# Optimization experiments

Hardware: AMD Instinct MI355X
Metric: run time of the kernel (lower is better)

Reference implementation:

```python
import jax, jax.numpy as jnp
import numpy as np

D_MODEL = 1024
D_HEAD = 128
BATCH = 4
SEQ = 4096


def setup_inputs() -> dict:
    key = jax.random.key(0)
    ks = jax.random.split(key, 7)
    s = 1.0 / np.sqrt(D_MODEL)
    return {
        "x": jax.random.normal(ks[0], (BATCH, SEQ, D_MODEL), dtype=jnp.float32),
        "Wq": jax.random.normal(ks[1], (D_MODEL, D_HEAD), dtype=jnp.float32) * s,
        "bq": jax.random.normal(ks[2], (D_HEAD,), dtype=jnp.float32) * 0.02,
        "Wk": jax.random.normal(ks[3], (D_MODEL, D_HEAD), dtype=jnp.float32) * s,
        "bk": jax.random.normal(ks[4], (D_HEAD,), dtype=jnp.float32) * 0.02,
        "Wv": jax.random.normal(ks[5], (D_MODEL, D_HEAD), dtype=jnp.float32) * s,
        "bv": jax.random.normal(ks[6], (D_HEAD,), dtype=jnp.float32) * 0.02,
    }


def reference(x, Wq, bq, Wk, bk, Wv, bv):
    # Single-head causal self-attention (intended math of MaskedAttention).
    # x: [B, S, D_MODEL]; projections to [B, S, D_HEAD].
    q = x @ Wq + bq
    k = x @ Wk + bk
    v = x @ Wv + bv
    scale = 1.0 / jnp.sqrt(jnp.asarray(D_HEAD, dtype=x.dtype))
    scores = jnp.einsum("bsd,btd->bst", q, k) * scale  # [B, S, S]
    # additive causal mask: -inf strictly above the diagonal
    s_len = scores.shape[-1]
    causal = jnp.tril(jnp.ones((s_len, s_len), dtype=bool))
    scores = jnp.where(causal[None, :, :], scores, jnp.asarray(-jnp.inf, dtype=scores.dtype))
    attn = jax.nn.softmax(scores, axis=-1)
    return jnp.einsum("bst,btd->bsd", attn, v)  # [B, S, D_HEAD]
```

## Files before the change

kernel.cpp:

```cpp
#include <hip/hip_runtime.h>
#include <stdint.h>
#include <stddef.h>

#define SEQ 4096
#define DM 1024
#define DH 128
#define NB 4
#define SPLITS 4

typedef __attribute__((ext_vector_type(8))) short bf16x8;
typedef __attribute__((ext_vector_type(4))) float f32x4;

__device__ __forceinline__ unsigned short f2bf(float f) {
    union { float f; uint32_t u; } v; v.f = f;
    uint32_t u = v.u + 0x7FFF + ((v.u >> 16) & 1);
    return (unsigned short)(u >> 16);
}

__device__ __forceinline__ void gload_lds16(const void* g, void* l) {
    __builtin_amdgcn_global_load_lds(
        (const __attribute__((address_space(1))) void*)g,
        (__attribute__((address_space(3))) void*)l, 16, 0, 0);
}

__global__ __launch_bounds__(256) void prep_kernel(
    const float* __restrict__ Wq, const float* __restrict__ Wk,
    const float* __restrict__ Wv, unsigned short* __restrict__ Wt)
{
    int idx = blockIdx.x * 256 + threadIdx.x;
    int n = idx >> 10, k = idx & 1023;
    int p = n >> 7, c = n & 127;
    const float* W = (p == 0) ? Wq : (p == 1) ? Wk : Wv;
    float v = W[k * DH + c];
    if (p == 0) v *= 0.08838834764831845f;
    Wt[idx] = f2bf(v);
}

__global__ __launch_bounds__(256) void proj_kernel(
    const float* __restrict__ x,
    const unsigned short* __restrict__ Wt,
    const float* __restrict__ bq, const float* __restrict__ bk,
    const float* __restrict__ bv,
    unsigned short* __restrict__ qb, unsigned short* __restrict__ kb,
    unsigned short* __restrict__ vt)
{
    __shared__ unsigned short A_lds[128 * 64];
    __shared__ unsigned short B_lds[128 * 64];
    const int tid = threadIdx.x;
    const int lane = tid & 63, w = tid >> 6;
    const int wr = w >> 1, wc = w & 1;
    const int q15 = lane & 15, g = lane >> 4;
    const int mt = blockIdx.x & 127, nt = blockIdx.x >> 7;

    f32x4 acc[4][4];
    #pragma unroll
    for (int i = 0; i < 4; ++i)
        #pragma unroll
        for (int j2 = 0; j2 < 4; ++j2) acc[i][j2] = (f32x4){0.f, 0.f, 0.f, 0.f};

    const int arow = tid >> 3, aseg = tid & 7;
    for (int kt = 0; kt < 16; ++kt) {
        #pragma unroll
        for (int i = 0; i < 4; ++i)
            gload_lds16(Wt + ((size_t)(nt * 128 + arow + i * 32) * DM + kt * 64 + aseg * 8),
                        (char*)B_lds + w * 1024 + i * 4096);
        #pragma unroll
        for (int rnd = 0; rnd < 4; ++rnd) {
            int chunk = rnd * 256 + tid;
            int row = chunk >> 3, seg = chunk & 7;
            const float* src = x + (size_t)(mt * 128 + row) * DM + kt * 64 + seg * 8;
            f32x4 lo4 = *(const f32x4*)src;
            f32x4 hi4 = *(const f32x4*)(src + 4);
            bf16x8 vv;
            vv[0] = (short)f2bf(lo4[0]); vv[1] = (short)f2bf(lo4[1]);
            vv[2] = (short)f2bf(lo4[2]); vv[3] = (short)f2bf(lo4[3]);
            vv[4] = (short)f2bf(hi4[0]); vv[5] = (short)f2bf(hi4[1]);
            vv[6] = (short)f2bf(hi4[2]); vv[7] = (short)f2bf(hi4[3]);
            *(bf16x8*)&A_lds[row * 64 + seg * 8] = vv;
        }
        __syncthreads();
        #pragma unroll
        for (int kk = 0; kk < 2; ++kk) {
            bf16x8 af[4], bfr[4];
            #pragma unroll
            for (int mi = 0; mi < 4; ++mi)
                af[mi] = *(const bf16x8*)&A_lds[(wr * 64 + mi * 16 + q15) * 64 + kk * 32 + g * 8];
            #pragma unroll
            for (int ni = 0; ni < 4; ++ni)
                bfr[ni] = *(const bf16x8*)&B_lds[(wc * 64 + ni * 16 + q15) * 64 + kk * 32 + g * 8];
            #pragma unroll
            for (int mi = 0; mi < 4; ++mi)
                #pragma unroll
                for (int ni = 0; ni < 4; ++ni)
                    acc[mi][ni] = __builtin_amdgcn_mfma_f32_16x16x32_bf16(
                        af[mi], bfr[ni], acc[mi][ni], 0, 0, 0);
        }
        __syncthreads();
    }
    const float* bias = (nt == 0) ? bq : (nt == 1) ? bk : bv;
    unsigned short* dst = (nt == 0) ? qb : kb;
    const float bscale = (nt == 0) ? 0.08838834764831845f : 1.0f;
    #pragma unroll
    for (int ni = 0; ni < 4; ++ni) {
        int nloc = wc * 64 + ni * 16 + q15;
        float bval = bias[nloc] * bscale;
        #pragma unroll
        for (int mi = 0; mi < 4; ++mi) {
            int m0 = mt * 128 + wr * 64 + mi * 16 + g * 4;
            #pragma unroll
            for (int r = 0; r < 4; ++r) {
                unsigned short h = f2bf(acc[mi][ni][r] + bval);
                int m = m0 + r;
                if (nt < 2) dst[(size_t)m * DH + nloc] = h;
                else {
                    int b = m >> 12, s = m & 4095;
                    vt[(size_t)(b * 128 + nloc) * SEQ + s] = h;
                }
            }
        }
    }
}

__global__ __launch_bounds__(512) void attn_kernel(
    const unsigned short* __restrict__ qb,
    const unsigned short* __restrict__ kb,
    const unsigned short* __restrict__ vt,
    float* __restrict__ po,
    float* __restrict__ pm, float* __restrict__ pl)
{
    __shared__ unsigned short K_lds[64 * 128];
    __shared__ unsigned short V_lds[128 * 64];
    __shared__ unsigned short P_lds[8 * 16 * 72];
    const int tid = threadIdx.x;
    const int w = tid >> 6;
    const int lane = tid & 63;
    const int q15 = lane & 15, g = lane >> 4;
    const int xcd = blockIdx.x & 7, slot = blockIdx.x >> 3;
    const int b = xcd >> 1;
    const int j = 31 - (slot >> 1);
    const int s = (slot & 1) * 2 + (xcd & 1);
    const int n = 2 * j + 2;
    const int lo = (n * s) >> 2, hi = (n * (s + 1)) >> 2;
    if (lo >= hi) return;
    const int qbase = j * 128;
    const int wq0 = qbase + w * 16;
    const int qglob = wq0 + q15;

    bf16x8 qf[4];
    const unsigned short* qrow = qb + (size_t)(b * SEQ + qglob) * DH;
    #pragma unroll
    for (int kk = 0; kk < 4; ++kk) qf[kk] = *(const bf16x8*)(qrow + kk * 32 + g * 8);

    f32x4 o[8];
    #pragma unroll
    for (int f = 0; f < 8; ++f) o[f] = (f32x4){0.f, 0.f, 0.f, 0.f};
    float m_run = -60.0f, l_run = 0.f;

    const unsigned short* Kb = kb + (size_t)b * SEQ * DH;
    const unsigned short* Vb = vt + (size_t)b * 128 * SEQ;
    unsigned short* Pw = &P_lds[w * 16 * 72];

    for (int kt = lo; kt < hi; ++kt) {
        {
            const unsigned short* Ksrc = Kb + (size_t)kt * 64 * DH;
            const unsigned short* Vsrc = Vb + kt * 64;
            #pragma unroll
            for (int i = 0; i < 2; ++i) {
                int krow = i * 32 + w * 4 + (lane >> 4);
                int kseg = (lane & 15) ^ (krow & 7);
                gload_lds16(Ksrc + (size_t)krow * DH + kseg * 8,
                            (char*)K_lds + i * 8192 + w * 1024);
                int vrow = i * 64 + w * 8 + (lane >> 3);
                int vseg = (lane & 7) ^ (vrow & 7);
                gload_lds16(Vsrc + (size_t)vrow * SEQ + vseg * 8,
                            (char*)V_lds + i * 8192 + w * 1024);
            }
        }
        __syncthreads();
        f32x4 sf[4];
        #pragma unroll
        for (int mt2 = 0; mt2 < 4; ++mt2) {
            f32x4 sa = (f32x4){0.f, 0.f, 0.f, 0.f};
            #pragma unroll
            for (int kk = 0; kk < 4; ++kk) {
                int seg = (kk * 4 + g) ^ (q15 & 7);
                bf16x8 kf = *(const bf16x8*)&K_lds[(mt2 * 16 + q15) * 128 + seg * 8];
                sa = __builtin_amdgcn_mfma_f32_16x16x32_bf16(kf, qf[kk], sa, 0, 0, 0);
            }
            sf[mt2] = sa;
        }
        float tmax = -__builtin_inff();
        if (kt * 64 + 63 > wq0) {
            #pragma unroll
            for (int mt2 = 0; mt2 < 4; ++mt2)
                #pragma unroll
                for (int r = 0; r < 4; ++r) {
                    int kglob = kt * 64 + mt2 * 16 + g * 4 + r;
                    float v = (kglob <= qglob) ? sf[mt2][r] : -__builtin_inff();
                    sf[mt2][r] = v;
                    tmax = fmaxf(tmax, v);
                }
        } else {
            #pragma unroll
            for (int mt2 = 0; mt2 < 4; ++mt2)
                #pragma unroll
                for (int r = 0; r < 4; ++r) tmax = fmaxf(tmax, sf[mt2][r]);
        }
        tmax = fmaxf(tmax, __shfl_xor(tmax, 16));
        tmax = fmaxf(tmax, __shfl_xor(tmax, 32));
        if (!__all((tmax - m_run) <= 8.0f)) {
            float m_new = fmaxf(m_run, tmax);
            float c = __expf(m_run - m_new);
            float cr[4];
            #pragma unroll
            for (int r = 0; r < 4; ++r) cr[r] = __shfl(c, g * 4 + r);
            #pragma unroll
            for (int f = 0; f < 8; ++f)
                #pragma unroll
                for (int r = 0; r < 4; ++r) o[f][r] *= cr[r];
            l_run *= c;
            m_run = m_new;
        }
        float rsum = 0.f;
        #pragma unroll
        for (int mt2 = 0; mt2 < 4; ++mt2)
            #pragma unroll
            for (int r = 0; r < 4; ++r) {
                float p = __expf(sf[mt2][r] - m_run);
                sf[mt2][r] = p;
                rsum += p;
            }
        rsum += __shfl_xor(rsum, 16);
        rsum += __shfl_xor(rsum, 32);
        l_run += rsum;
        uint32_t* pbase = (uint32_t*)&Pw[q15 * 72];
        #pragma unroll
        for (int mt2 = 0; mt2 < 4; ++mt2) {
            uint32_t p01 = (uint32_t)f2bf(sf[mt2][0]) | ((uint32_t)f2bf(sf[mt2][1]) << 16);
            uint32_t p23 = (uint32_t)f2bf(sf[mt2][2]) | ((uint32_t)f2bf(sf[mt2][3]) << 16);
            int e = mt2 * 16 + g * 4;
            pbase[e >> 1] = p01;
            pbase[(e >> 1) + 1] = p23;
        }
        asm volatile("s_waitcnt lgkmcnt(0)" ::: "memory");
        bf16x8 pf[2];
        #pragma unroll
        for (int kk2 = 0; kk2 < 2; ++kk2)
            pf[kk2] = *(const bf16x8*)&Pw[q15 * 72 + kk2 * 32 + g * 8];
        #pragma unroll
        for (int f = 0; f < 8; ++f) {
            #pragma unroll
            for (int kk2 = 0; kk2 < 2; ++kk2) {
                int seg = (kk2 * 4 + g) ^ (q15 & 7);
                bf16x8 vf = *(const bf16x8*)&V_lds[(f * 16 + q15) * 64 + seg * 8];
                o[f] = __builtin_amdgcn_mfma_f32_16x16x32_bf16(pf[kk2], vf, o[f], 0, 0, 0);
            }
        }
        __syncthreads();
    }
    float* pob = po + ((size_t)(s * NB + b) * SEQ + wq0) * DH;
    #pragma unroll
    for (int f = 0; f < 8; ++f)
        #pragma unroll
        for (int r = 0; r < 4; ++r)
            pob[(size_t)(g * 4 + r) * DH + f * 16 + q15] = o[f][r];
    if (g == 0) {
        size_t sidx = (size_t)(s * NB + b) * SEQ + wq0 + q15;
        pm[sidx] = m_run;
        pl[sidx] = l_run;
    }
}

__global__ __launch_bounds__(256) void reduce_kernel(
    const float* __restrict__ po, const float* __restrict__ pm,
    const float* __restrict__ pl, float* __restrict__ out)
{
    int r = blockIdx.x * 8 + (threadIdx.x >> 5);
    int d0 = (threadIdx.x & 31) * 4;
    int b = r >> 12, q = r & 4095;
    int n = 2 * (q >> 7) + 2;
    float ms[SPLITS];
    float M = -__builtin_inff();
    #pragma unroll
    for (int s = 0; s < SPLITS; ++s) {
        int lo = (n * s) >> 2, hi = (n * (s + 1)) >> 2;
        if (hi > lo) {
            ms[s] = pm[(size_t)(s * NB + b) * SEQ + q];
            M = fmaxf(M, ms[s]);
        } else ms[s] = -__builtin_inff();
    }
    float L = 0.f;
    f32x4 acc = (f32x4){0.f, 0.f, 0.f, 0.f};
    #pragma unroll
    for (int s = 0; s < SPLITS; ++s) {
        int lo = (n * s) >> 2, hi = (n * (s + 1)) >> 2;
        if (hi > lo) {
            float wgt = __expf(ms[s] - M);
            L += wgt * pl[(size_t)(s * NB + b) * SEQ + q];
            f32x4 p = *(const f32x4*)&po[((size_t)(s * NB + b) * SEQ + q) * DH + d0];
            acc += wgt * p;
        }
    }
    float inv = 1.0f / L;
    *(f32x4*)&out[((size_t)(b * SEQ) + q) * DH + d0] = acc * inv;
}

extern "C" void kernel_launch(void* const* d_in, const int* in_sizes, int n_in,
                              void* d_out, int out_size, void* d_ws, size_t ws_size,
                              hipStream_t stream)
{
    const float* x  = (const float*)d_in[0];
    const float* Wq = (const float*)d_in[1];
    const float* bq = (const float*)d_in[2];
    const float* Wk = (const float*)d_in[3];
    const float* bk = (const float*)d_in[4];
    const float* Wv = (const float*)d_in[5];
    const float* bv = (const float*)d_in[6];

    char* ws = (char*)d_ws;
    unsigned short* Wt = (unsigned short*)(ws + 33554432);
    unsigned short* qb = (unsigned short*)(ws + 34340864);
    unsigned short* kb = (unsigned short*)(ws + 38535168);
    unsigned short* vt = (unsigned short*)(ws + 42729472);
    float* po = (float*)(ws);
    float* pm = (float*)(ws + 33554432);
    float* pl = (float*)(ws + 33554432 + 262144);

    prep_kernel<<<1536, 256, 0, stream>>>(Wq, Wk, Wv, Wt);
    proj_kernel<<<384, 256, 0, stream>>>(x, Wt, bq, bk, bv, qb, kb, vt);
    attn_kernel<<<512, 512, 0, stream>>>(qb, kb, vt, po, pm, pl);
    reduce_kernel<<<2048, 256, 0, stream>>>(po, pm, pl, (float*)d_out);
}
```

Measured before the change: 188.1 us.

## Fuse QKV projection into one 64x384 tile per block with double-buffered LDS

The projection kernel now computes all of Q, K and V for a 64-row slab of x in a single block of 512 threads, instead of three separate blocks per 128-row slab. Each block reads and converts x to bf16 once rather than three times. The kernel also double-buffers both A and B tiles in LDS, prefetching the next k-slice while MFMAs run. The B tile uses an XOR swizzle and the A tile uses padding to avoid LDS bank conflicts. The cost is a larger LDS footprint (about 116KB) and fewer blocks (256), which may limit occupancy on a 256-CU part.

Measured after the change: 177.1 us. -5.9%, faster.

```diff
diff --git a/kernel.cpp b/kernel.cpp
--- a/kernel.cpp
+++ b/kernel.cpp
@@ -36,7 +36,7 @@
     Wt[idx] = f2bf(v);
 }
 
-__global__ __launch_bounds__(256) void proj_kernel(
+__global__ __launch_bounds__(512) void proj_kernel(
     const float* __restrict__ x,
     const unsigned short* __restrict__ Wt,
     const float* __restrict__ bq, const float* __restrict__ bk,
@@ -44,78 +44,101 @@
     unsigned short* __restrict__ qb, unsigned short* __restrict__ kb,
     unsigned short* __restrict__ vt)
 {
-    __shared__ unsigned short A_lds[128 * 64];
-    __shared__ unsigned short B_lds[128 * 64];
+    __shared__ unsigned short A_lds[2][64 * 72];
+    __shared__ unsigned short B_lds[2][384 * 64];
     const int tid = threadIdx.x;
     const int lane = tid & 63, w = tid >> 6;
-    const int wr = w >> 1, wc = w & 1;
+    const int wm = w >> 2, wn = w & 3;
     const int q15 = lane & 15, g = lane >> 4;
-    const int mt = blockIdx.x & 127, nt = blockIdx.x >> 7;
-
-    f32x4 acc[4][4];
-    #pragma unroll
-    for (int i = 0; i < 4; ++i)
-        #pragma unroll
-        for (int j2 = 0; j2 < 4; ++j2) acc[i][j2] = (f32x4){0.f, 0.f, 0.f, 0.f};
+    const int mt = blockIdx.x;
 
     const int arow = tid >> 3, aseg = tid & 7;
+
+    f32x4 acc[2][6];
+    #pragma unroll
+    for (int mi = 0; mi < 2; ++mi)
+        #pragma unroll
+        for (int ni = 0; ni < 6; ++ni) acc[mi][ni] = (f32x4){0.f, 0.f, 0.f, 0.f};
+
+    const float* asrc = x + (size_t)(mt * 64 + arow) * DM + aseg * 8;
+
+    #pragma unroll
+    for (int t = 0; t < 6; ++t) {
+        int brow = t * 64 + arow;
+        int bl = aseg ^ (brow & 7);
+        gload_lds16(Wt + (size_t)brow * DM + bl * 8,
+                    (char*)&B_lds[0][0] + t * 8192 + tid * 16);
+    }
+    {
+        f32x4 lo4 = *(const f32x4*)asrc;
+        f32x4 hi4 = *(const f32x4*)(asrc + 4);
+        bf16x8 vv;
+        vv[0] = (short)f2bf(lo4[0]); vv[1] = (short)f2bf(lo4[1]);
+        vv[2] = (short)f2bf(lo4[2]); vv[3] = (short)f2bf(lo4[3]);
+        vv[4] = (short)f2bf(hi4[0]); vv[5] = (short)f2bf(hi4[1]);
+        vv[6] = (short)f2bf(hi4[2]); vv[7] = (short)f2bf(hi4[3]);
+        *(bf16x8*)&A_lds[0][arow * 72 + aseg * 8] = vv;
+    }
+    __syncthreads();
+
+    int cur = 0;
     for (int kt = 0; kt < 16; ++kt) {
-        #pragma unroll
-        for (int i = 0; i < 4; ++i)
-            gload_lds16(Wt + ((size_t)(nt * 128 + arow + i * 32) * DM + kt * 64 + aseg * 8),
-                        (char*)B_lds + w * 1024 + i * 4096);
-        #pragma unroll
-        for (int rnd = 0; rnd < 4; ++rnd) {
-            int chunk = rnd * 256 + tid;
-            int row = chunk >> 3, seg = chunk & 7;
-            const float* src = x + (size_t)(mt * 128 + row) * DM + kt * 64 + seg * 8;
-            f32x4 lo4 = *(const f32x4*)src;
-            f32x4 hi4 = *(const f32x4*)(src + 4);
-            bf16x8 vv;
-            vv[0] = (short)f2bf(lo4[0]); vv[1] = (short)f2bf(lo4[1]);
-            vv[2] = (short)f2bf(lo4[2]); vv[3] = (short)f2bf(lo4[3]);
-            vv[4] = (short)f2bf(hi4[0]); vv[5] = (short)f2bf(hi4[1]);
-            vv[6] = (short)f2bf(hi4[2]); vv[7] = (short)f2bf(hi4[3]);
-            *(bf16x8*)&A_lds[row * 64 + seg * 8] = vv;
-        }
-        __syncthreads();
+        f32x4 nlo, nhi;
+        if (kt < 15) {
+            #pragma unroll
+            for (int t = 0; t < 6; ++t) {
+                int brow = t * 64 + arow;
+                int bl = aseg ^ (brow & 7);
+                gload_lds16(Wt + (size_t)brow * DM + (kt + 1) * 64 + bl * 8,
+                            (char*)&B_lds[cur ^ 1][0] + t * 8192 + tid * 16);
+            }
+            nlo = *(const f32x4*)(asrc + (kt + 1) * 64);
+            nhi = *(const f32x4*)(asrc + (kt + 1) * 64 + 4);
+        }
         #pragma unroll
         for (int kk = 0; kk < 2; ++kk) {
-            bf16x8 af[4], bfr[4];
-            #pragma unroll
-            for (int mi = 0; mi < 4; ++mi)
-                af[mi] = *(const bf16x8*)&A_lds[(wr * 64 + mi * 16 + q15) * 64 + kk * 32 + g * 8];
-            #pragma unroll
-            for (int ni = 0; ni < 4; ++ni)
-                bfr[ni] = *(const bf16x8*)&B_lds[(wc * 64 + ni * 16 + q15) * 64 + kk * 32 + g * 8];
-            #pragma unroll
-            for (int mi = 0; mi < 4; ++mi)
+            bf16x8 af[2], bfr[6];
+            #pragma unroll
+            for (int mi = 0; mi < 2; ++mi)
+                af[mi] = *(const bf16x8*)&A_lds[cur][(wm * 32 + mi * 16 + q15) * 72 + (kk * 4 + g) * 8];
+            #pragma unroll
+            for (int ni = 0; ni < 6; ++ni)
+                bfr[ni] = *(const bf16x8*)&B_lds[cur][(wn * 96 + ni * 16 + q15) * 64 + ((kk * 4 + g) ^ (q15 & 7)) * 8];
+            #pragma unroll
+            for (int mi = 0; mi < 2; ++mi)
                 #pragma unroll
-                for (int ni = 0; ni < 4; ++ni)
+                for (int ni = 0; ni < 6; ++ni)
                     acc[mi][ni] = __builtin_amdgcn_mfma_f32_16x16x32_bf16(
                         af[mi], bfr[ni], acc[mi][ni], 0, 0, 0);
         }
+        if (kt < 15) {
+            bf16x8 vv;
+            vv[0] = (short)f2bf(nlo[0]); vv[1] = (short)f2bf(nlo[1]);
+            vv[2] = (short)f2bf(nlo[2]); vv[3] = (short)f2bf(nlo[3]);
+            vv[4] = (short)f2bf(nhi[0]); vv[5] = (short)f2bf(nhi[1]);
+            vv[6] = (short)f2bf(nhi[2]); vv[7] = (short)f2bf(nhi[3]);
+            *(bf16x8*)&A_lds[cur ^ 1][arow * 72 + aseg * 8] = vv;
+        }
         __syncthreads();
-    }
-    const float* bias = (nt == 0) ? bq : (nt == 1) ? bk : bv;
-    unsigned short* dst = (nt == 0) ? qb : kb;
-    const float bscale = (nt == 0) ? 0.08838834764831845f : 1.0f;
-    #pragma unroll
-    for (int ni = 0; ni < 4; ++ni) {
-        int nloc = wc * 64 + ni * 16 + q15;
-        float bval = bias[nloc] * bscale;
-        #pragma unroll
-        for (int mi = 0; mi < 4; ++mi) {
-            int m0 = mt * 128 + wr * 64 + mi * 16 + g * 4;
+        cur ^= 1;
+    }
+
+    #pragma unroll
+    for (int ni = 0; ni < 6; ++ni) {
+        int n = wn * 96 + ni * 16 + q15;
+        int p = n >> 7, c = n & 127;
+        const float* bias = (p == 0) ? bq : (p == 1) ? bk : bv;
+        float bval = bias[c] * ((p == 0) ? 0.08838834764831845f : 1.0f);
+        #pragma unroll
+        for (int mi = 0; mi < 2; ++mi) {
+            int m0 = mt * 64 + wm * 32 + mi * 16 + g * 4;
             #pragma unroll
             for (int r = 0; r < 4; ++r) {
                 unsigned short h = f2bf(acc[mi][ni][r] + bval);
                 int m = m0 + r;
-                if (nt < 2) dst[(size_t)m * DH + nloc] = h;
-                else {
-                    int b = m >> 12, s = m & 4095;
-                    vt[(size_t)(b * 128 + nloc) * SEQ + s] = h;
-                }
+                if (p == 0) qb[(size_t)m * DH + c] = h;
+                else if (p == 1) kb[(size_t)m * DH + c] = h;
+                else vt[(size_t)((m >> 12) * 128 + c) * SEQ + (m & 4095)] = h;
             }
         }
     }
@@ -327,7 +350,7 @@
     float* pl = (float*)(ws + 33554432 + 262144);
 
     prep_kernel<<<1536, 256, 0, stream>>>(Wq, Wk, Wv, Wt);
-    proj_kernel<<<384, 256, 0, stream>>>(x, Wt, bq, bk, bv, qb, kb, vt);
+    proj_kernel<<<256, 512, 0, stream>>>(x, Wt, bq, bk, bv, qb, kb, vt);
     attn_kernel<<<512, 512, 0, stream>>>(qb, kb, vt, po, pm, pl);
     reduce_kernel<<<2048, 256, 0, stream>>>(po, pm, pl, (float*)d_out);
 }
```
